# Performance work log

Measured on AMD Instinct MI355X. Metric: run time of the kernel, lower is better.

The kernel has to match this reference:

```python
import jax, jax.numpy as jnp
import numpy as np

M = 4        # modalities
T = 4096     # events per modality
D = 64       # d_qk + 2
NLIN = 3     # n_layers=2 hidden -> 3 linear layers per MLP


def _make_x(k, T, D):
    kx, kt = jax.random.split(k)
    x = jax.random.normal(kx, (1, 1, T, D), dtype=jnp.float32)
    # last feature channel holds sorted event timestamps
    t = jnp.sort(jax.random.uniform(kt, (T,), dtype=jnp.float32))
    return x.at[0, 0, :, -1].set(t)


def setup_inputs() -> dict:
    key = jax.random.key(0)
    ks = jax.random.split(key, M + 4)
    xs = [_make_x(ks[m], T, D) for m in range(M)]
    Wq_w = 0.05 * jax.random.normal(ks[M], (NLIN, D, D), dtype=jnp.float32)
    Wq_b = jnp.zeros((NLIN, D), dtype=jnp.float32)
    Wk_w = 0.05 * jax.random.normal(ks[M + 1], (M, NLIN, D, D), dtype=jnp.float32)
    Wk_b = jnp.zeros((M, NLIN, D), dtype=jnp.float32)
    return {"x1": xs[0], "x2": xs[1], "x3": xs[2], "x4": xs[3],
            "Wq_w": Wq_w, "Wq_b": Wq_b, "Wk_w": Wk_w, "Wk_b": Wk_b}


def mlp(x, Ws, bs):
    # stack of (D,D) linears, relu between layers (not after final)
    h = x
    n = Ws.shape[0]
    for i in range(n):
        h = h @ Ws[i] + bs[i]
        if i < n - 1:
            h = jax.nn.relu(h)
    return h


def reference(x1, x2, x3, x4, Wq_w, Wq_b, Wk_w, Wk_b):
    Q = mlp(x1, Wq_w, Wq_b)[0, 0]          # (T1, D)
    t1 = x1[0, 0, :, -1]                    # query timestamps
    acc = jnp.zeros((Q.shape[0], 2), dtype=Q.dtype)
    for m, xm in enumerate((x1, x2, x3, x4)):  # fixed small modality set
        K = mlp(xm, Wk_w[m], Wk_b[m])[0, 0]    # (T2, D)
        V = xm[0, 0]                            # (T2, D), V = X
        t2 = xm[0, 0, :, -1]
        # timestamp-causal mask: key j visible to query i iff t2[j] <= t1[i]
        mask = (t2[None, :] <= t1[:, None]).astype(Q.dtype)  # (T1, T2)
        out_m = ((Q @ K.T) * mask) @ V          # causal dot-product, (T1, D)
        acc = acc + out_m[:, :2]                # Zout.sum(1)[..., :2]
    return acc[None]                            # (1, T1, 2)
```

## Files before the change

### kernel.cpp

```cpp
#include <hip/hip_runtime.h>

#define TT 4096
#define DD 64
#define NCH2 128
#define CS2 32

#define Q_OFF    0
#define K_OFF    (TT*DD)
#define Z_OFF    (K_OFF + 4*TT*DD)
#define CSUM_OFF (Z_OFF + 8*TT*DD)
#define T_OFF    (CSUM_OFF + 8*NCH2*DD)

__global__ __launch_bounds__(512, 4) void mlp_kernel(
    const float* __restrict__ x1, const float* __restrict__ x2,
    const float* __restrict__ x3, const float* __restrict__ x4,
    const float* __restrict__ Wq_w, const float* __restrict__ Wq_b,
    const float* __restrict__ Wk_w, const float* __restrict__ Wk_b,
    float* __restrict__ ws)
{
    const int q    = blockIdx.x >> 6;
    const int br   = blockIdx.x & 63;
    const int lane = threadIdx.x & 63;
    const int w    = threadIdx.x >> 6;

    const float* x; const float* W; const float* B; float* out;
    if (q == 0) { x = x1; W = Wq_w; B = Wq_b; out = ws + Q_OFF; }
    else {
        const int m = q - 1;
        x = (m == 0) ? x1 : (m == 1) ? x2 : (m == 2) ? x3 : x4;
        W = Wk_w + m * 3 * DD * DD;
        B = Wk_b + m * 3 * DD;
        out = ws + K_OFF + m * TT * DD;
    }

    __shared__ float hs[DD * DD];
    __shared__ float vb[2 * DD];

    {
        const float4* xv = reinterpret_cast<const float4*>(x + br * 64 * DD);
        #pragma unroll
        for (int half = 0; half < 2; ++half) {
            const int idx = threadIdx.x + half * 512;
            const float4 v = xv[idx];
            const int e   = idx * 4;
            const int row = e >> 6;
            const int k0  = e & 63;
            const int slot = ((k0 >> 2) ^ (row & 7)) << 2;
            *reinterpret_cast<float4*>(&hs[row * 64 + slot]) = v;
            if (k0 == 0)  { vb[row] = v.x; vb[DD + row] = v.y; }
            if (q >= 1 && k0 == 60) ws[T_OFF + (q - 1) * TT + br * 64 + row] = v.w;
        }
    }

    const int dofs = __builtin_amdgcn_readfirstlane(8 * w);
    const int r3   = lane & 7;

    float h[DD];
    float a[8];

    for (int L = 0; L < 3; ++L) {
        __syncthreads();

        #pragma unroll
        for (int g = 0; g < 16; ++g) {
            const float4 hv = *reinterpret_cast<const float4*>(&hs[lane * 64 + ((g ^ r3) << 2)]);
            h[4*g + 0] = hv.x; h[4*g + 1] = hv.y;
            h[4*g + 2] = hv.z; h[4*g + 3] = hv.w;
        }

        const float* WL = W + L * DD * DD + dofs;
        const float* BL = B + L * DD + dofs;
        {
            const float4 b0 = *reinterpret_cast<const float4*>(BL);
            const float4 b1 = *reinterpret_cast<const float4*>(BL + 4);
            a[0] = b0.x; a[1] = b0.y; a[2] = b0.z; a[3] = b0.w;
            a[4] = b1.x; a[5] = b1.y; a[6] = b1.z; a[7] = b1.w;
        }

        #pragma unroll
        for (int k = 0; k < DD; ++k) {
            const float hk = h[k];
            const float4 wa = *reinterpret_cast<const float4*>(WL + k * DD);
            const float4 wb = *reinterpret_cast<const float4*>(WL + k * DD + 4);
            a[0] += hk * wa.x; a[1] += hk * wa.y; a[2] += hk * wa.z; a[3] += hk * wa.w;
            a[4] += hk * wb.x; a[5] += hk * wb.y; a[6] += hk * wb.z; a[7] += hk * wb.w;
        }

        if (L < 2) {
            #pragma unroll
            for (int j = 0; j < 8; ++j) a[j] = fmaxf(a[j], 0.f);
            __syncthreads();
            const int g0 = 2 * w;
            *reinterpret_cast<float4*>(&hs[lane * 64 + ((g0 ^ r3) << 2)]) =
                make_float4(a[0], a[1], a[2], a[3]);
            *reinterpret_cast<float4*>(&hs[lane * 64 + (((g0 + 1) ^ r3) << 2)]) =
                make_float4(a[4], a[5], a[6], a[7]);
        }
    }

    {
        float* o = out + (br * 64 + lane) * DD + dofs;
        *reinterpret_cast<float4*>(o)     = make_float4(a[0], a[1], a[2], a[3]);
        *reinterpret_cast<float4*>(o + 4) = make_float4(a[4], a[5], a[6], a[7]);
    }

    if (q >= 1) {
        const int m = q - 1;
        const float v0 = vb[lane], v1 = vb[DD + lane];
        float p0[8], p1[8];
        #pragma unroll
        for (int j = 0; j < 8; ++j) { p0[j] = a[j] * v0; p1[j] = a[j] * v1; }
        #pragma unroll
        for (int off = 1; off <= 16; off <<= 1) {
            #pragma unroll
            for (int j = 0; j < 8; ++j) {
                p0[j] += __shfl_xor(p0[j], off);
                p1[j] += __shfl_xor(p1[j], off);
            }
        }
        if ((lane & 31) == 0) {
            const int ch2 = br * 2 + (lane >> 5);
            float* c0 = ws + CSUM_OFF + ((m * 2 + 0) * NCH2 + ch2) * DD + dofs;
            float* c1 = ws + CSUM_OFF + ((m * 2 + 1) * NCH2 + ch2) * DD + dofs;
            #pragma unroll
            for (int j = 0; j < 8; ++j) { c0[j] = p0[j]; c1[j] = p1[j]; }
        }
    }
}

__global__ __launch_bounds__(64) void zfill_kernel(
    const float* __restrict__ x1, const float* __restrict__ x2,
    const float* __restrict__ x3, const float* __restrict__ x4,
    float* __restrict__ ws)
{
    const int mc  = blockIdx.x >> 7;
    const int ch2 = blockIdx.x & 127;
    const int m   = mc >> 1;
    const int c   = mc & 1;
    const int d   = threadIdx.x;
    const float* xm = (m == 0) ? x1 : (m == 1) ? x2 : (m == 2) ? x3 : x4;
    const float* K = ws + K_OFF + m * TT * DD;
    const float* csum = ws + CSUM_OFF + mc * NCH2 * DD;
    float* Z = ws + Z_OFF + mc * TT * DD;

    float r = 0.f;
    #pragma unroll
    for (int cc = 0; cc < NCH2 - 1; ++cc) {
        const float v = csum[cc * DD + d];
        r += (cc < ch2) ? v : 0.f;
    }

    const int j0 = ch2 * CS2;
    #pragma unroll 8
    for (int jj = 0; jj < CS2; ++jj) {
        const int j = j0 + jj;
        r += K[j * DD + d] * xm[j * DD + c];
        Z[j * DD + d] = r;
    }
}

__global__ __launch_bounds__(256) void gather_kernel(
    const float* __restrict__ ws, float* __restrict__ out)
{
    const int lane = threadIdx.x & 63;
    const int wid  = threadIdx.x >> 6;
    const int i = blockIdx.x * 4 + wid;

    const float* Q  = ws + Q_OFF;
    const float* Z  = ws + Z_OFF;
    const float* tb = ws + T_OFF;

    const float t1i = tb[0 * TT + i];
    const float qd  = Q[i * DD + lane];

    int lo[4] = {0, 0, 0, 0};
    int hi[4] = {TT, TT, TT, TT};
    #pragma unroll
    for (int s = 0; s < 13; ++s) {
        #pragma unroll
        for (int m = 0; m < 4; ++m) {
            if (lo[m] < hi[m]) {
                const int mid = (lo[m] + hi[m]) >> 1;
                const bool le = tb[m * TT + mid] <= t1i;
                lo[m] = le ? mid + 1 : lo[m];
                hi[m] = le ? hi[m] : mid;
            }
        }
    }

    float a0 = 0.f, a1 = 0.f;
    #pragma unroll
    for (int m = 0; m < 4; ++m) {
        if (lo[m] > 0) {
            const int p = lo[m] - 1;
            a0 += qd * Z[((m * 2 + 0) * TT + p) * DD + lane];
            a1 += qd * Z[((m * 2 + 1) * TT + p) * DD + lane];
        }
    }

    #pragma unroll
    for (int off = 32; off > 0; off >>= 1) {
        a0 += __shfl_xor(a0, off);
        a1 += __shfl_xor(a1, off);
    }
    if (lane == 0) {
        out[i * 2 + 0] = a0;
        out[i * 2 + 1] = a1;
    }
}

extern "C" void kernel_launch(void* const* d_in, const int* in_sizes, int n_in,
                              void* d_out, int out_size, void* d_ws, size_t ws_size,
                              hipStream_t stream)
{
    const float* x1   = (const float*)d_in[0];
    const float* x2   = (const float*)d_in[1];
    const float* x3   = (const float*)d_in[2];
    const float* x4   = (const float*)d_in[3];
    const float* Wq_w = (const float*)d_in[4];
    const float* Wq_b = (const float*)d_in[5];
    const float* Wk_w = (const float*)d_in[6];
    const float* Wk_b = (const float*)d_in[7];
    float* out = (float*)d_out;
    float* ws  = (float*)d_ws;

    hipLaunchKernelGGL(mlp_kernel,   dim3(5 * 64), dim3(512), 0, stream,
                       x1, x2, x3, x4, Wq_w, Wq_b, Wk_w, Wk_b, ws);
    hipLaunchKernelGGL(zfill_kernel, dim3(8 * NCH2), dim3(64), 0, stream,
                       x1, x2, x3, x4, ws);
    hipLaunchKernelGGL(gather_kernel, dim3(TT / 4), dim3(256), 0, stream,
                       ws, out);
}
```

Before: 51.27 us.

## Replace full prefix-sum materialization with chunk scan plus per-query partial sums

Drops the kernel that wrote the full 8×T×D cumulative K·V tensor. The MLP kernel now stores per-16-row chunk sums and the first two V columns. A tiny 8-block kernel turns the chunk sums into an exclusive scan, and the output kernel adds the scanned prefix to up to 16 K·V terms per query. This removes roughly 8 MB of Z writes and reads, but adds a serial 256-step scan in a single wave per block and a variable-length inner loop in the output kernel.

```diff
diff --git a/kernel.cpp b/kernel.cpp
--- a/kernel.cpp
+++ b/kernel.cpp
@@ -2,14 +2,14 @@
 
 #define TT 4096
 #define DD 64
-#define NCH2 128
-#define CS2 32
+#define NCH3 256
+#define CS3 16
 
 #define Q_OFF    0
 #define K_OFF    (TT*DD)
-#define Z_OFF    (K_OFF + 4*TT*DD)
-#define CSUM_OFF (Z_OFF + 8*TT*DD)
-#define T_OFF    (CSUM_OFF + 8*NCH2*DD)
+#define CSUM_OFF (K_OFF + 4*TT*DD)
+#define V_OFF    (CSUM_OFF + 8*NCH3*DD)
+#define T_OFF    (V_OFF + 8*TT)
 
 __global__ __launch_bounds__(512, 4) void mlp_kernel(
     const float* __restrict__ x1, const float* __restrict__ x2,
@@ -47,7 +47,13 @@
             const int k0  = e & 63;
             const int slot = ((k0 >> 2) ^ (row & 7)) << 2;
             *reinterpret_cast<float4*>(&hs[row * 64 + slot]) = v;
-            if (k0 == 0)  { vb[row] = v.x; vb[DD + row] = v.y; }
+            if (k0 == 0) {
+                vb[row] = v.x; vb[DD + row] = v.y;
+                if (q >= 1) {
+                    float* vp = ws + V_OFF + ((q - 1) * TT + br * 64 + row) * 2;
+                    vp[0] = v.x; vp[1] = v.y;
+                }
+            }
             if (q >= 1 && k0 == 60) ws[T_OFF + (q - 1) * TT + br * 64 + row] = v.w;
         }
     }
@@ -111,55 +117,38 @@
         #pragma unroll
         for (int j = 0; j < 8; ++j) { p0[j] = a[j] * v0; p1[j] = a[j] * v1; }
         #pragma unroll
-        for (int off = 1; off <= 16; off <<= 1) {
+        for (int off = 1; off <= 8; off <<= 1) {
             #pragma unroll
             for (int j = 0; j < 8; ++j) {
                 p0[j] += __shfl_xor(p0[j], off);
                 p1[j] += __shfl_xor(p1[j], off);
             }
         }
-        if ((lane & 31) == 0) {
-            const int ch2 = br * 2 + (lane >> 5);
-            float* c0 = ws + CSUM_OFF + ((m * 2 + 0) * NCH2 + ch2) * DD + dofs;
-            float* c1 = ws + CSUM_OFF + ((m * 2 + 1) * NCH2 + ch2) * DD + dofs;
+        if ((lane & 15) == 0) {
+            const int ch3 = br * 4 + (lane >> 4);
+            float* c0 = ws + CSUM_OFF + ((m * 2 + 0) * NCH3 + ch3) * DD + dofs;
+            float* c1 = ws + CSUM_OFF + ((m * 2 + 1) * NCH3 + ch3) * DD + dofs;
             #pragma unroll
             for (int j = 0; j < 8; ++j) { c0[j] = p0[j]; c1[j] = p1[j]; }
         }
     }
 }
 
-__global__ __launch_bounds__(64) void zfill_kernel(
-    const float* __restrict__ x1, const float* __restrict__ x2,
-    const float* __restrict__ x3, const float* __restrict__ x4,
-    float* __restrict__ ws)
-{
-    const int mc  = blockIdx.x >> 7;
-    const int ch2 = blockIdx.x & 127;
-    const int m   = mc >> 1;
-    const int c   = mc & 1;
-    const int d   = threadIdx.x;
-    const float* xm = (m == 0) ? x1 : (m == 1) ? x2 : (m == 2) ? x3 : x4;
-    const float* K = ws + K_OFF + m * TT * DD;
-    const float* csum = ws + CSUM_OFF + mc * NCH2 * DD;
-    float* Z = ws + Z_OFF + mc * TT * DD;
-
-    float r = 0.f;
-    #pragma unroll
-    for (int cc = 0; cc < NCH2 - 1; ++cc) {
-        const float v = csum[cc * DD + d];
-        r += (cc < ch2) ? v : 0.f;
-    }
-
-    const int j0 = ch2 * CS2;
+__global__ __launch_bounds__(64) void scan_kernel(float* __restrict__ ws)
+{
+    const int mc = blockIdx.x;
+    const int d  = threadIdx.x;
+    float* c = ws + CSUM_OFF + mc * NCH3 * DD + d;
+    float run = 0.f;
     #pragma unroll 8
-    for (int jj = 0; jj < CS2; ++jj) {
-        const int j = j0 + jj;
-        r += K[j * DD + d] * xm[j * DD + c];
-        Z[j * DD + d] = r;
-    }
-}
-
-__global__ __launch_bounds__(256) void gather_kernel(
+    for (int ch = 0; ch < NCH3; ++ch) {
+        const float v = c[ch * DD];
+        c[ch * DD] = run;
+        run += v;
+    }
+}
+
+__global__ __launch_bounds__(256) void out_kernel(
     const float* __restrict__ ws, float* __restrict__ out)
 {
     const int lane = threadIdx.x & 63;
@@ -167,7 +156,6 @@
     const int i = blockIdx.x * 4 + wid;
 
     const float* Q  = ws + Q_OFF;
-    const float* Z  = ws + Z_OFF;
     const float* tb = ws + T_OFF;
 
     const float t1i = tb[0 * TT + i];
@@ -188,16 +176,28 @@
         }
     }
 
-    float a0 = 0.f, a1 = 0.f;
+    float g0 = 0.f, g1 = 0.f;
     #pragma unroll
     for (int m = 0; m < 4; ++m) {
         if (lo[m] > 0) {
-            const int p = lo[m] - 1;
-            a0 += qd * Z[((m * 2 + 0) * TT + p) * DD + lane];
-            a1 += qd * Z[((m * 2 + 1) * TT + p) * DD + lane];
-        }
-    }
-
+            const int p    = lo[m] - 1;
+            const int ch   = p >> 4;
+            const int base = ch << 4;
+            const float* c0 = ws + CSUM_OFF + ((m * 2 + 0) * NCH3 + ch) * DD;
+            const float* c1 = ws + CSUM_OFF + ((m * 2 + 1) * NCH3 + ch) * DD;
+            g0 += c0[lane];
+            g1 += c1[lane];
+            const float* K  = ws + K_OFF + m * TT * DD;
+            const float* V2 = ws + V_OFF + m * TT * 2;
+            for (int j = base; j <= p; ++j) {
+                const float kv = K[j * DD + lane];
+                g0 += kv * V2[j * 2 + 0];
+                g1 += kv * V2[j * 2 + 1];
+            }
+        }
+    }
+
+    float a0 = qd * g0, a1 = qd * g1;
     #pragma unroll
     for (int off = 32; off > 0; off >>= 1) {
         a0 += __shfl_xor(a0, off);
@@ -224,10 +224,9 @@
     float* out = (float*)d_out;
     float* ws  = (float*)d_ws;
 
-    hipLaunchKernelGGL(mlp_kernel,   dim3(5 * 64), dim3(512), 0, stream,
+    hipLaunchKernelGGL(mlp_kernel,  dim3(5 * 64), dim3(512), 0, stream,
                        x1, x2, x3, x4, Wq_w, Wq_b, Wk_w, Wk_b, ws);
-    hipLaunchKernelGGL(zfill_kernel, dim3(8 * NCH2), dim3(64), 0, stream,
-                       x1, x2, x3, x4, ws);
-    hipLaunchKernelGGL(gather_kernel, dim3(TT / 4), dim3(256), 0, stream,
+    hipLaunchKernelGGL(scan_kernel, dim3(8), dim3(64), 0, stream, ws);
+    hipLaunchKernelGGL(out_kernel,  dim3(TT / 4), dim3(256), 0, stream,
                        ws, out);
 }
```

New measurement: 61.15 us. +19.3%, slower.

## Run MLP layers on bf16x3 MFMA with pre-packed split weights

Applied to the files above, without the earlier changes.

Replaces the scalar FP32 FMA MLP kernel with a matrix-core version. Weights and activations are split into bf16 high and low halves, and three MFMA products are summed to approximate FP32 accuracy. A new small kernel packs the weights into MFMA operand layout on every call, and row blocks shrink to 32 rows with 128 threads. This adds an extra kernel launch and some accuracy risk from dropping the low×low term, in exchange for far less ALU work in the MLP stage.

```diff
diff --git a/kernel.cpp b/kernel.cpp
--- a/kernel.cpp
+++ b/kernel.cpp
@@ -1,4 +1,8 @@
 #include <hip/hip_runtime.h>
+
+typedef __attribute__((ext_vector_type(8))) short bf16x8;
+typedef __attribute__((ext_vector_type(4))) float f32x4;
+typedef __attribute__((ext_vector_type(4))) unsigned int u32x4;
 
 #define TT 4096
 #define DD 64
@@ -10,121 +14,170 @@
 #define Z_OFF    (K_OFF + 4*TT*DD)
 #define CSUM_OFF (Z_OFF + 8*TT*DD)
 #define T_OFF    (CSUM_OFF + 8*NCH2*DD)
-
-__global__ __launch_bounds__(512, 4) void mlp_kernel(
+#define WP_OFF   (T_OFF + 4*TT)
+#define WP_HALF  61440
+
+__global__ __launch_bounds__(256) void wpack_kernel(
+    const float* __restrict__ Wq_w, const float* __restrict__ Wk_w,
+    float* __restrict__ ws)
+{
+    const int ell = blockIdx.x;
+    const int q = ell / 3, L = ell % 3;
+    const float* Wsrc = (q == 0) ? (Wq_w + L * DD * DD)
+                                 : (Wk_w + ((q - 1) * 3 + L) * DD * DD);
+    unsigned short* wp = reinterpret_cast<unsigned short*>(ws + WP_OFF);
+    for (int idx = threadIdx.x; idx < 4096; idx += 256) {
+        const int j = idx & 7;
+        const int l = (idx >> 3) & 63;
+        const int n = (idx >> 9) & 3;
+        const int t = (idx >> 11) & 1;
+        const int k = t * 32 + (l >> 4) * 8 + j;
+        const int c = n * 16 + (l & 15);
+        const float wv = Wsrc[k * DD + c];
+        const unsigned int u = __float_as_uint(wv);
+        const unsigned short hi = (unsigned short)(u >> 16);
+        const float hif = __uint_as_float(((unsigned int)hi) << 16);
+        const float lof = wv - hif;
+        const unsigned int v = __float_as_uint(lof);
+        const unsigned short lo = (unsigned short)((v + 0x7FFFu + ((v >> 16) & 1u)) >> 16);
+        const int dst = (((ell * 2 + t) * 4 + n) * 64 + l) * 8 + j;
+        wp[dst] = hi;
+        wp[WP_HALF + dst] = lo;
+    }
+}
+
+__global__ __launch_bounds__(128) void mlpmm_kernel(
     const float* __restrict__ x1, const float* __restrict__ x2,
     const float* __restrict__ x3, const float* __restrict__ x4,
-    const float* __restrict__ Wq_w, const float* __restrict__ Wq_b,
-    const float* __restrict__ Wk_w, const float* __restrict__ Wk_b,
+    const float* __restrict__ Wq_b, const float* __restrict__ Wk_b,
     float* __restrict__ ws)
 {
-    const int q    = blockIdx.x >> 6;
-    const int br   = blockIdx.x & 63;
-    const int lane = threadIdx.x & 63;
-    const int w    = threadIdx.x >> 6;
-
-    const float* x; const float* W; const float* B; float* out;
-    if (q == 0) { x = x1; W = Wq_w; B = Wq_b; out = ws + Q_OFF; }
+    const int q   = blockIdx.x >> 7;
+    const int rb  = blockIdx.x & 127;
+    const int tid = threadIdx.x;
+    const int l   = tid & 63;
+    const int w   = tid >> 6;
+
+    const float* x; const float* Bsrc; float* out;
+    if (q == 0) { x = x1; Bsrc = Wq_b; out = ws + Q_OFF; }
     else {
         const int m = q - 1;
         x = (m == 0) ? x1 : (m == 1) ? x2 : (m == 2) ? x3 : x4;
-        W = Wk_w + m * 3 * DD * DD;
-        B = Wk_b + m * 3 * DD;
+        Bsrc = Wk_b + m * 3 * DD;
         out = ws + K_OFF + m * TT * DD;
     }
 
-    __shared__ float hs[DD * DD];
-    __shared__ float vb[2 * DD];
+    __shared__ float hs[32 * 68];
+    __shared__ float vb[2 * 32];
+    __shared__ float ps[2][2][64];
 
     {
-        const float4* xv = reinterpret_cast<const float4*>(x + br * 64 * DD);
-        #pragma unroll
-        for (int half = 0; half < 2; ++half) {
-            const int idx = threadIdx.x + half * 512;
+        const float4* xv = reinterpret_cast<const float4*>(x + rb * 32 * DD);
+        #pragma unroll
+        for (int i = 0; i < 4; ++i) {
+            const int idx = tid + i * 128;
             const float4 v = xv[idx];
-            const int e   = idx * 4;
-            const int row = e >> 6;
-            const int k0  = e & 63;
-            const int slot = ((k0 >> 2) ^ (row & 7)) << 2;
-            *reinterpret_cast<float4*>(&hs[row * 64 + slot]) = v;
-            if (k0 == 0)  { vb[row] = v.x; vb[DD + row] = v.y; }
-            if (q >= 1 && k0 == 60) ws[T_OFF + (q - 1) * TT + br * 64 + row] = v.w;
-        }
-    }
-
-    const int dofs = __builtin_amdgcn_readfirstlane(8 * w);
-    const int r3   = lane & 7;
-
-    float h[DD];
-    float a[8];
+            const int e = idx * 4;
+            const int row = e >> 6, k0 = e & 63;
+            *reinterpret_cast<float4*>(&hs[row * 68 + k0]) = v;
+            if (k0 == 0) { vb[row] = v.x; vb[32 + row] = v.y; }
+            if (q >= 1 && k0 == 60) ws[T_OFF + (q - 1) * TT + rb * 32 + row] = v.w;
+        }
+    }
+    __syncthreads();
+
+    const unsigned short* wp = reinterpret_cast<const unsigned short*>(ws + WP_OFF);
+    const int lane15 = l & 15, lhi = l >> 4;
+    const int wrow = w * 16;
 
     for (int L = 0; L < 3; ++L) {
+        bf16x8 bh[2][4], bl[2][4];
+        #pragma unroll
+        for (int t = 0; t < 2; ++t) {
+            #pragma unroll
+            for (int n = 0; n < 4; ++n) {
+                const int f = ((((q * 3 + L) * 2 + t) * 4 + n) * 64 + l) * 8;
+                bh[t][n] = *reinterpret_cast<const bf16x8*>(wp + f);
+                bl[t][n] = *reinterpret_cast<const bf16x8*>(wp + WP_HALF + f);
+            }
+        }
+
+        bf16x8 ah[2], al[2];
+        #pragma unroll
+        for (int t = 0; t < 2; ++t) {
+            const float* src = &hs[(wrow + lane15) * 68 + t * 32 + lhi * 8];
+            float x8[8];
+            *reinterpret_cast<float4*>(&x8[0]) = *reinterpret_cast<const float4*>(src);
+            *reinterpret_cast<float4*>(&x8[4]) = *reinterpret_cast<const float4*>(src + 4);
+            unsigned int hw[4], lw[4];
+            #pragma unroll
+            for (int p = 0; p < 4; ++p) {
+                const unsigned int u0 = __float_as_uint(x8[2*p]);
+                const unsigned int u1 = __float_as_uint(x8[2*p+1]);
+                const unsigned int h0 = u0 >> 16, h1 = u1 >> 16;
+                const float f0 = x8[2*p]   - __uint_as_float(h0 << 16);
+                const float f1 = x8[2*p+1] - __uint_as_float(h1 << 16);
+                const unsigned int v0 = __float_as_uint(f0), v1 = __float_as_uint(f1);
+                const unsigned int l0 = (v0 + 0x7FFFu + ((v0 >> 16) & 1u)) >> 16;
+                const unsigned int l1 = (v1 + 0x7FFFu + ((v1 >> 16) & 1u)) >> 16;
+                hw[p] = h0 | (h1 << 16);
+                lw[p] = l0 | (l1 << 16);
+            }
+            const u32x4 hv = {hw[0], hw[1], hw[2], hw[3]};
+            const u32x4 lv = {lw[0], lw[1], lw[2], lw[3]};
+            ah[t] = __builtin_bit_cast(bf16x8, hv);
+            al[t] = __builtin_bit_cast(bf16x8, lv);
+        }
+
+        f32x4 acc[4];
+        #pragma unroll
+        for (int n = 0; n < 4; ++n) acc[n] = (f32x4){0.f, 0.f, 0.f, 0.f};
+
+        #pragma unroll
+        for (int t = 0; t < 2; ++t) {
+            #pragma unroll
+            for (int n = 0; n < 4; ++n) {
+                acc[n] = __builtin_amdgcn_mfma_f32_16x16x32_bf16(ah[t], bh[t][n], acc[n], 0, 0, 0);
+                acc[n] = __builtin_amdgcn_mfma_f32_16x16x32_bf16(ah[t], bl[t][n], acc[n], 0, 0, 0);
+                acc[n] = __builtin_amdgcn_mfma_f32_16x16x32_bf16(al[t], bh[t][n], acc[n], 0, 0, 0);
+            }
+        }
+
+        #pragma unroll
+        for (int n = 0; n < 4; ++n) {
+            const float bv = Bsrc[L * DD + n * 16 + lane15];
+            #pragma unroll
+            for (int r = 0; r < 4; ++r) {
+                float val = acc[n][r] + bv;
+                if (L < 2) val = fmaxf(val, 0.f);
+                hs[(wrow + lhi * 4 + r) * 68 + n * 16 + lane15] = val;
+            }
+        }
+    }
+
+    #pragma unroll
+    for (int rr = 0; rr < 16; ++rr) {
+        out[(rb * 32 + wrow + rr) * DD + l] = hs[(wrow + rr) * 68 + l];
+    }
+
+    if (q >= 1) {
         __syncthreads();
-
-        #pragma unroll
-        for (int g = 0; g < 16; ++g) {
-            const float4 hv = *reinterpret_cast<const float4*>(&hs[lane * 64 + ((g ^ r3) << 2)]);
-            h[4*g + 0] = hv.x; h[4*g + 1] = hv.y;
-            h[4*g + 2] = hv.z; h[4*g + 3] = hv.w;
-        }
-
-        const float* WL = W + L * DD * DD + dofs;
-        const float* BL = B + L * DD + dofs;
-        {
-            const float4 b0 = *reinterpret_cast<const float4*>(BL);
-            const float4 b1 = *reinterpret_cast<const float4*>(BL + 4);
-            a[0] = b0.x; a[1] = b0.y; a[2] = b0.z; a[3] = b0.w;
-            a[4] = b1.x; a[5] = b1.y; a[6] = b1.z; a[7] = b1.w;
-        }
-
-        #pragma unroll
-        for (int k = 0; k < DD; ++k) {
-            const float hk = h[k];
-            const float4 wa = *reinterpret_cast<const float4*>(WL + k * DD);
-            const float4 wb = *reinterpret_cast<const float4*>(WL + k * DD + 4);
-            a[0] += hk * wa.x; a[1] += hk * wa.y; a[2] += hk * wa.z; a[3] += hk * wa.w;
-            a[4] += hk * wb.x; a[5] += hk * wb.y; a[6] += hk * wb.z; a[7] += hk * wb.w;
-        }
-
-        if (L < 2) {
-            #pragma unroll
-            for (int j = 0; j < 8; ++j) a[j] = fmaxf(a[j], 0.f);
-            __syncthreads();
-            const int g0 = 2 * w;
-            *reinterpret_cast<float4*>(&hs[lane * 64 + ((g0 ^ r3) << 2)]) =
-                make_float4(a[0], a[1], a[2], a[3]);
-            *reinterpret_cast<float4*>(&hs[lane * 64 + (((g0 + 1) ^ r3) << 2)]) =
-                make_float4(a[4], a[5], a[6], a[7]);
-        }
-    }
-
-    {
-        float* o = out + (br * 64 + lane) * DD + dofs;
-        *reinterpret_cast<float4*>(o)     = make_float4(a[0], a[1], a[2], a[3]);
-        *reinterpret_cast<float4*>(o + 4) = make_float4(a[4], a[5], a[6], a[7]);
-    }
-
-    if (q >= 1) {
         const int m = q - 1;
-        const float v0 = vb[lane], v1 = vb[DD + lane];
-        float p0[8], p1[8];
-        #pragma unroll
-        for (int j = 0; j < 8; ++j) { p0[j] = a[j] * v0; p1[j] = a[j] * v1; }
-        #pragma unroll
-        for (int off = 1; off <= 16; off <<= 1) {
-            #pragma unroll
-            for (int j = 0; j < 8; ++j) {
-                p0[j] += __shfl_xor(p0[j], off);
-                p1[j] += __shfl_xor(p1[j], off);
-            }
-        }
-        if ((lane & 31) == 0) {
-            const int ch2 = br * 2 + (lane >> 5);
-            float* c0 = ws + CSUM_OFF + ((m * 2 + 0) * NCH2 + ch2) * DD + dofs;
-            float* c1 = ws + CSUM_OFF + ((m * 2 + 1) * NCH2 + ch2) * DD + dofs;
-            #pragma unroll
-            for (int j = 0; j < 8; ++j) { c0[j] = p0[j]; c1[j] = p1[j]; }
-        }
+        const int d = tid & 63;
+        const int g = tid >> 6;
+        float p0 = 0.f, p1 = 0.f;
+        #pragma unroll
+        for (int rr = 0; rr < 16; ++rr) {
+            const int row = g * 16 + rr;
+            const float kv = hs[row * 68 + d];
+            p0 += kv * vb[row];
+            p1 += kv * vb[32 + row];
+        }
+        ps[g][0][d] = p0; ps[g][1][d] = p1;
+        __syncthreads();
+        const int c = g;
+        const float s = ps[0][c][d] + ps[1][c][d];
+        ws[CSUM_OFF + ((m * 2 + c) * NCH2 + rb) * DD + d] = s;
     }
 }
 
@@ -224,8 +277,10 @@
     float* out = (float*)d_out;
     float* ws  = (float*)d_ws;
 
-    hipLaunchKernelGGL(mlp_kernel,   dim3(5 * 64), dim3(512), 0, stream,
-                       x1, x2, x3, x4, Wq_w, Wq_b, Wk_w, Wk_b, ws);
+    hipLaunchKernelGGL(wpack_kernel, dim3(15), dim3(256), 0, stream,
+                       Wq_w, Wk_w, ws);
+    hipLaunchKernelGGL(mlpmm_kernel, dim3(5 * 128), dim3(128), 0, stream,
+                       x1, x2, x3, x4, Wq_b, Wk_b, ws);
     hipLaunchKernelGGL(zfill_kernel, dim3(8 * NCH2), dim3(64), 0, stream,
                        x1, x2, x3, x4, ws);
     hipLaunchKernelGGL(gather_kernel, dim3(TT / 4), dim3(256), 0, stream,
```

Measured after the change: 42.12 us, median of 2. 17.9% less time.
